# Performance work log

Measured on AMD Instinct MI355X. Metric: run time of the kernel, lower is better.

The kernel has to match this reference:

```python
import jax, jax.numpy as jnp
import numpy as np
import math

NUM_LEVELS = 16
LEVEL_DIM = 2
BASE_RES = 16
MAX_RES = 2048
HASHMAP_SIZE = 1 << 19  # 2**log2_hashmap_size
B, N = 4, 262144


def setup_inputs() -> dict:
    key = jax.random.key(0)
    k1, k2 = jax.random.split(key)
    x = jax.random.uniform(k1, (B, N, 3), dtype=jnp.float32)  # coords in [0,1]
    # per-level hash tables, init uniform(-1e-4, 1e-4) as in the torch module
    embeddings = jax.random.uniform(
        k2, (NUM_LEVELS, HASHMAP_SIZE, LEVEL_DIM),
        minval=-1e-4, maxval=1e-4, dtype=jnp.float32)
    return {"x": x, "embeddings": embeddings}


def reference(x, embeddings):
    # per_level_scale = exp((ln(max)-ln(base))/(L-1))
    per_level_scale = math.exp((math.log(MAX_RES) - math.log(BASE_RES)) / (NUM_LEVELS - 1))
    H = HASHMAP_SIZE
    feats = []
    for level in range(NUM_LEVELS):
        res = int(BASE_RES * per_level_scale ** level)  # static per level
        # floor coords, wrap into [0, res)
        cf = jnp.floor(x * res).astype(jnp.int32) % res  # [B,N,3]
        # hash = (c0 + c1*res + c2*res^2) mod H, computed in modular arithmetic
        # so everything fits in int32 (max term ~2047 * (2^19-1) < 2^31).
        h = (cf[..., 0] % H
             + (cf[..., 1] * res) % H
             + (cf[..., 2] * ((res * res) % H)) % H) % H  # [B,N]
        feats.append(embeddings[level][h])  # gather -> [B,N,LEVEL_DIM]
    return jnp.concatenate(feats, axis=-1)  # [B,N,NUM_LEVELS*LEVEL_DIM]
```

## Files before the change

### kernel.cpp

```cpp
#include <hip/hip_runtime.h>
#include <cmath>

#define NLEVELS 16
#define HSIZE   (1 << 19)
#define HMASK   (HSIZE - 1)

typedef float v2f __attribute__((ext_vector_type(2)));
typedef float v4f __attribute__((ext_vector_type(4)));

struct LevelParams {
    int res[NLEVELS];
    int r2mod[NLEVELS];
};

__device__ __forceinline__ int hash_one(float x0, float x1, float x2, int res, int r2)
{
    const float fr = (float)res;
    int c0 = (int)floorf(x0 * fr); if (c0 >= res) c0 -= res;
    int c1 = (int)floorf(x1 * fr); if (c1 >= res) c1 -= res;
    int c2 = (int)floorf(x2 * fr); if (c2 >= res) c2 -= res;
    return (c0 + ((c1 * res) & HMASK) + ((c2 * r2) & HMASK)) & HMASK;
}

#define K1_PPT   4
#define K1_CHUNK (256 * K1_PPT)

__global__ __launch_bounds__(256)
void hashgrid_gather2(const float* __restrict__ x,
                      const float* __restrict__ emb,
                      v2f* __restrict__ ws,
                      LevelParams lp, int npts, int blocksA)
{
    __shared__ float sx[K1_CHUNK * 3];
    const int tid = threadIdx.x;

    int level, base, end;
    if ((int)blockIdx.x < blocksA) {
        const int g = blockIdx.x & 7;
        level = 5 + g;
        base  = (int)(blockIdx.x >> 3) * K1_CHUNK;
        end   = npts;
        if (base >= npts) return;
    } else {
        const int idx = (int)blockIdx.x - blocksA;
        const int g   = idx & 7;
        int shard, nsh;
        if (g < 3)      { level = 13; shard = g;     nsh = 3; }
        else if (g < 6) { level = 14; shard = g - 3; nsh = 3; }
        else            { level = 15; shard = g - 6; nsh = 2; }
        const int shardN = (npts + nsh - 1) / nsh;
        base = shard * shardN + (idx >> 3) * K1_CHUNK;
        end  = min(npts, (shard + 1) * shardN);
        if (base >= end) return;
    }

    const int nfl = npts * 3;
    const int b3  = base * 3;
    #pragma unroll
    for (int k = 0; k < 3 * K1_PPT; ++k) {
        const int idx = b3 + tid + k * 256;
        if (idx < nfl) sx[tid + k * 256] = __builtin_nontemporal_load(&x[idx]);
    }
    __syncthreads();

    const int res = lp.res[level];
    const int r2  = lp.r2mod[level];
    const v2f* __restrict__ e2 = (const v2f*)emb + (size_t)level * HSIZE;
    v2f* __restrict__ wl = ws + (size_t)level * npts;

    v2f v[K1_PPT];
    int pg[K1_PPT];
    #pragma unroll
    for (int k = 0; k < K1_PPT; ++k) {
        const int pl = tid + k * 256;
        const int p  = base + pl;
        pg[k] = p;
        if (p < end) {
            const int h = hash_one(sx[pl * 3], sx[pl * 3 + 1], sx[pl * 3 + 2], res, r2);
            v[k] = e2[h];
        }
    }
    #pragma unroll
    for (int k = 0; k < K1_PPT; ++k)
        if (pg[k] < end)
            __builtin_nontemporal_store(v[k], &wl[pg[k]]);
}

__global__ __launch_bounds__(256)
void hashgrid_finalize(const float* __restrict__ x,
                       const float* __restrict__ emb,
                       const v2f* __restrict__ ws,
                       v4f* __restrict__ out4,
                       LevelParams lp, int npts)
{
    __shared__ float sx[768];
    __shared__ v2f   sl[16][257];

    const int tid = threadIdx.x;
    const int p0  = (int)blockIdx.x * 256;

    const int nfl = npts * 3;
    const int b3  = p0 * 3;
    #pragma unroll
    for (int k = 0; k < 3; ++k) {
        const int idx = b3 + tid + k * 256;
        if (idx < nfl) sx[tid + k * 256] = __builtin_nontemporal_load(&x[idx]);
    }
    __syncthreads();

    const int  p     = p0 + tid;
    const bool valid = (p < npts);
    const v2f* __restrict__ e2 = (const v2f*)emb;

    const float x0 = sx[tid * 3 + 0];
    const float x1 = sx[tid * 3 + 1];
    const float x2 = sx[tid * 3 + 2];

    v2f g[5];
    #pragma unroll
    for (int l = 0; l < 5; ++l) {
        g[l] = valid
             ? e2[(size_t)l * HSIZE + hash_one(x0, x1, x2, lp.res[l], lp.r2mod[l])]
             : (v2f)(0.0f);
    }
    v2f r[11];
    #pragma unroll
    for (int li = 0; li < 11; ++li) {
        r[li] = valid
              ? __builtin_nontemporal_load(&ws[(size_t)(5 + li) * npts + p])
              : (v2f)(0.0f);
    }

    #pragma unroll
    for (int l = 0; l < 5; ++l)  sl[l][tid]      = g[l];
    #pragma unroll
    for (int li = 0; li < 11; ++li) sl[5 + li][tid] = r[li];
    __syncthreads();

    const int j  = tid & 7;
    const int tq = tid >> 3;

    #pragma unroll
    for (int k = 0; k < 8; ++k) {
        const int pp = k * 32 + tq;
        if (p0 + pp < npts) {
            const v2f va = sl[2 * j][pp];
            const v2f vb = sl[2 * j + 1][pp];
            v4f o; o.x = va.x; o.y = va.y; o.z = vb.x; o.w = vb.y;
            __builtin_nontemporal_store(o, &out4[(size_t)p0 * 8 + k * 256 + tid]);
        }
    }
}

__global__ __launch_bounds__(256)
void hashgrid_fwd(const float* __restrict__ x,
                  const float* __restrict__ emb,
                  float* __restrict__ out,
                  LevelParams lp, int npts)
{
    __shared__ float sx[256 * 3];
    const int tid        = threadIdx.x;
    const int block_base = blockIdx.x * 256;
    const int nfl        = npts * 3;
    const int base3      = block_base * 3;
    #pragma unroll
    for (int k = 0; k < 3; ++k) {
        int idx = base3 + tid + k * 256;
        if (idx < nfl) sx[tid + k * 256] = x[idx];
    }
    __syncthreads();
    const int p = block_base + tid;
    if (p >= npts) return;
    const float x0 = sx[tid * 3 + 0], x1 = sx[tid * 3 + 1], x2 = sx[tid * 3 + 2];
    const float2* __restrict__ e2 = (const float2*)emb;
    float2 v[NLEVELS];
    #pragma unroll
    for (int l = 0; l < NLEVELS; ++l) {
        const int h = hash_one(x0, x1, x2, lp.res[l], lp.r2mod[l]);
        v[l] = e2[(size_t)l * HSIZE + h];
    }
    float4* __restrict__ o4 = (float4*)(out + (size_t)p * (NLEVELS * 2));
    #pragma unroll
    for (int i = 0; i < 8; ++i)
        o4[i] = make_float4(v[2 * i].x, v[2 * i].y, v[2 * i + 1].x, v[2 * i + 1].y);
}

extern "C" void kernel_launch(void* const* d_in, const int* in_sizes, int n_in,
                              void* d_out, int out_size, void* d_ws, size_t ws_size,
                              hipStream_t stream)
{
    const float* x   = (const float*)d_in[0];
    const float* emb = (const float*)d_in[1];
    float*       out = (float*)d_out;

    const int npts = in_sizes[0] / 3;

    LevelParams lp;
    const double s = std::exp((std::log(2048.0) - std::log(16.0)) / 15.0);
    for (int l = 0; l < NLEVELS; ++l) {
        const double r = 16.0 * std::pow(s, (double)l);
        const int res  = (int)r;
        lp.res[l]   = res;
        lp.r2mod[l] = (int)(((long long)res * res) % HSIZE);
    }

    const size_t ws_need = (size_t)NLEVELS * (size_t)npts * sizeof(v2f);
    if (ws_size >= ws_need) {
        const int cA      = (npts + K1_CHUNK - 1) / K1_CHUNK;
        const int blocksA = cA * 8;
        const int shardN2 = (npts + 1) / 2;
        const int cB      = (shardN2 + K1_CHUNK - 1) / K1_CHUNK;
        const int grid1   = blocksA + cB * 8;
        hipLaunchKernelGGL(hashgrid_gather2, dim3(grid1), dim3(256), 0, stream,
                           x, emb, (v2f*)d_ws, lp, npts, blocksA);
        const int grid2 = (npts + 255) / 256;
        hipLaunchKernelGGL(hashgrid_finalize, dim3(grid2), dim3(256), 0, stream,
                           x, emb, (const v2f*)d_ws, (v4f*)out, lp, npts);
    } else {
        const int blocks = (npts + 255) / 256;
        hipLaunchKernelGGL(hashgrid_fwd, dim3(blocks), dim3(256), 0, stream,
                           x, emb, out, lp, npts);
    }
}
```

Baseline: 337.9 us.

## Double points per thread in gather, vectorize coord loads, drop LDS staging in finalize

Raises points per thread in the gather kernel from 4 to 8, so each block issues more independent random embedding loads and fewer blocks are launched. Shard boundaries are rounded to chunk multiples so that float4 coordinate loads stay aligned. The coordinate staging into shared memory now uses float4 loads in place of scalar nontemporal loads. The finalize kernel drops its shared-memory coordinate staging and barrier, issues the workspace loads first, and reads coordinates directly with strided per-thread loads. The cost is higher register pressure in the gather kernel and uncoalesced coordinate reads in finalize.

```diff
diff --git a/kernel.cpp b/kernel.cpp
--- a/kernel.cpp
+++ b/kernel.cpp
@@ -22,7 +22,7 @@
     return (c0 + ((c1 * res) & HMASK) + ((c2 * r2) & HMASK)) & HMASK;
 }
 
-#define K1_PPT   4
+#define K1_PPT   8
 #define K1_CHUNK (256 * K1_PPT)
 
 __global__ __launch_bounds__(256)
@@ -48,7 +48,7 @@
         if (g < 3)      { level = 13; shard = g;     nsh = 3; }
         else if (g < 6) { level = 14; shard = g - 3; nsh = 3; }
         else            { level = 15; shard = g - 6; nsh = 2; }
-        const int shardN = (npts + nsh - 1) / nsh;
+        const int shardN = (((npts + nsh - 1) / nsh + K1_CHUNK - 1) / K1_CHUNK) * K1_CHUNK;
         base = shard * shardN + (idx >> 3) * K1_CHUNK;
         end  = min(npts, (shard + 1) * shardN);
         if (base >= end) return;
@@ -56,10 +56,21 @@
 
     const int nfl = npts * 3;
     const int b3  = base * 3;
-    #pragma unroll
-    for (int k = 0; k < 3 * K1_PPT; ++k) {
-        const int idx = b3 + tid + k * 256;
-        if (idx < nfl) sx[tid + k * 256] = __builtin_nontemporal_load(&x[idx]);
+    {
+        const float4* __restrict__ x4 = (const float4*)(x + b3);
+        float4* __restrict__ sx4 = (float4*)sx;
+        #pragma unroll
+        for (int k = 0; k < (3 * K1_PPT) / 4; ++k) {
+            const int e  = tid + k * 256;
+            const int f0 = b3 + e * 4;
+            if (f0 + 3 < nfl) {
+                sx4[e] = x4[e];
+            } else {
+                #pragma unroll
+                for (int j = 0; j < 4; ++j)
+                    if (f0 + j < nfl) sx[e * 4 + j] = x[f0 + j];
+            }
+        }
     }
     __syncthreads();
 
@@ -69,21 +80,20 @@
     v2f* __restrict__ wl = ws + (size_t)level * npts;
 
     v2f v[K1_PPT];
-    int pg[K1_PPT];
     #pragma unroll
     for (int k = 0; k < K1_PPT; ++k) {
         const int pl = tid + k * 256;
-        const int p  = base + pl;
-        pg[k] = p;
-        if (p < end) {
+        if (base + pl < end) {
             const int h = hash_one(sx[pl * 3], sx[pl * 3 + 1], sx[pl * 3 + 2], res, r2);
             v[k] = e2[h];
         }
     }
     #pragma unroll
-    for (int k = 0; k < K1_PPT; ++k)
-        if (pg[k] < end)
-            __builtin_nontemporal_store(v[k], &wl[pg[k]]);
+    for (int k = 0; k < K1_PPT; ++k) {
+        const int p = base + tid + k * 256;
+        if (p < end)
+            __builtin_nontemporal_store(v[k], &wl[p]);
+    }
 }
 
 __global__ __launch_bounds__(256)
@@ -93,36 +103,13 @@
                        v4f* __restrict__ out4,
                        LevelParams lp, int npts)
 {
-    __shared__ float sx[768];
-    __shared__ v2f   sl[16][257];
+    __shared__ v2f sl[16][257];
 
     const int tid = threadIdx.x;
     const int p0  = (int)blockIdx.x * 256;
-
-    const int nfl = npts * 3;
-    const int b3  = p0 * 3;
-    #pragma unroll
-    for (int k = 0; k < 3; ++k) {
-        const int idx = b3 + tid + k * 256;
-        if (idx < nfl) sx[tid + k * 256] = __builtin_nontemporal_load(&x[idx]);
-    }
-    __syncthreads();
-
     const int  p     = p0 + tid;
     const bool valid = (p < npts);
-    const v2f* __restrict__ e2 = (const v2f*)emb;
-
-    const float x0 = sx[tid * 3 + 0];
-    const float x1 = sx[tid * 3 + 1];
-    const float x2 = sx[tid * 3 + 2];
-
-    v2f g[5];
-    #pragma unroll
-    for (int l = 0; l < 5; ++l) {
-        g[l] = valid
-             ? e2[(size_t)l * HSIZE + hash_one(x0, x1, x2, lp.res[l], lp.r2mod[l])]
-             : (v2f)(0.0f);
-    }
+
     v2f r[11];
     #pragma unroll
     for (int li = 0; li < 11; ++li) {
@@ -131,8 +118,20 @@
               : (v2f)(0.0f);
     }
 
-    #pragma unroll
-    for (int l = 0; l < 5; ++l)  sl[l][tid]      = g[l];
+    const float x0 = valid ? x[p * 3 + 0] : 0.0f;
+    const float x1 = valid ? x[p * 3 + 1] : 0.0f;
+    const float x2 = valid ? x[p * 3 + 2] : 0.0f;
+
+    v2f g[5];
+    #pragma unroll
+    for (int l = 0; l < 5; ++l) {
+        g[l] = valid
+             ? ((const v2f*)emb)[(size_t)l * HSIZE + hash_one(x0, x1, x2, lp.res[l], lp.r2mod[l])]
+             : (v2f)(0.0f);
+    }
+
+    #pragma unroll
+    for (int l = 0; l < 5; ++l)     sl[l][tid]      = g[l];
     #pragma unroll
     for (int li = 0; li < 11; ++li) sl[5 + li][tid] = r[li];
     __syncthreads();
@@ -208,7 +207,7 @@
     if (ws_size >= ws_need) {
         const int cA      = (npts + K1_CHUNK - 1) / K1_CHUNK;
         const int blocksA = cA * 8;
-        const int shardN2 = (npts + 1) / 2;
+        const int shardN2 = (((npts + 1) / 2 + K1_CHUNK - 1) / K1_CHUNK) * K1_CHUNK;
         const int cB      = (shardN2 + K1_CHUNK - 1) / K1_CHUNK;
         const int grid1   = blocksA + cB * 8;
         hipLaunchKernelGGL(hashgrid_gather2, dim3(grid1), dim3(256), 0, stream,
```

Measured after the change: 315.6 us. 1.07x faster.
